# Performance work log

Hardware: AMD Instinct MI355X
Metric: run time of the kernel (lower is better)

The kernel has to match this reference:

```python
import jax, jax.numpy as jnp
import numpy as np

N_NODES = 50000
E = 800000
NODE_NF = 128
EDGE_NF = 64
IN_NF = NODE_NF + EDGE_NF  # 192
H_NF = 256
OUT_NF = 128


def setup_inputs() -> dict:
    key = jax.random.key(0)
    k1, k2, k3, k4, k5 = jax.random.split(key, 5)
    node_feats = jax.random.normal(k1, (N_NODES, NODE_NF), dtype=jnp.float32)
    edge_index = jax.random.randint(k2, (2, E), 0, N_NODES, dtype=jnp.int64)
    edge_attr = jax.random.normal(k3, (E, EDGE_NF), dtype=jnp.float32)
    # MLP params (Linear stores weight [out, in]; we keep [in, out] for x @ W)
    s1 = 1.0 / np.sqrt(IN_NF)
    s2 = 1.0 / np.sqrt(H_NF)
    W1 = jax.random.uniform(k4, (IN_NF, H_NF), minval=-s1, maxval=s1, dtype=jnp.float32)
    b1 = jnp.zeros((H_NF,), dtype=jnp.float32)
    W2 = jax.random.uniform(k5, (H_NF, OUT_NF), minval=-s2, maxval=s2, dtype=jnp.float32)
    b2 = jnp.zeros((OUT_NF,), dtype=jnp.float32)
    return {"node_feats": node_feats, "edge_index": edge_index, "edge_attr": edge_attr,
            "W1": W1, "b1": b1, "W2": W2, "b2": b2}


def reference(node_feats, edge_index, edge_attr, W1, b1, W2, b2):
    row = edge_index[0]
    # unsorted_segment_sum: scatter-add edge_attr rows into per-node buckets
    agg = jax.ops.segment_sum(edge_attr, row, num_segments=node_feats.shape[0])  # [N, edge_nf]
    node_in = jnp.concatenate([node_feats, agg], axis=1)  # [N, in_nf]
    h = jax.nn.relu(node_in @ W1 + b1)
    return h @ W2 + b2
```

## Files before the change

kernel.cpp:

```cpp
#include <hip/hip_runtime.h>
#include <hip/hip_bf16.h>

typedef unsigned short u16;
typedef unsigned int u32;
typedef __attribute__((ext_vector_type(8))) short short8;
typedef __attribute__((ext_vector_type(4))) float floatx4;

#define N_NODES 50000
#define E_EDGES 800000
#define NODE_NF 128
#define EDGE_NF 64
#define IN_NF 192
#define H_NF 256
#define OUT_NF 128
#define CAP 64

__device__ __forceinline__ float bf2f(u16 u) {
    union { u32 i; float f; } v;
    v.i = ((u32)u) << 16;
    return v.f;
}

__device__ __forceinline__ u16 f2bf(float f) {
    union { float f; u32 i; } v;
    v.f = f;
    u32 b = v.i + 0x7FFF + ((v.i >> 16) & 1);
    return (u16)(b >> 16);
}

__global__ void probe_kernel(const u32* __restrict__ nf, const u32* __restrict__ ea,
                             const u32* __restrict__ w1, const int* __restrict__ eidx,
                             int* __restrict__ flags) {
    if (threadIdx.x != 0 || blockIdx.x != 0) return;
    int cn = 0, ce = 0, cw = 0;
    for (int i = 0; i < 64; ++i) {
        u32 bn = (nf[i] >> 8) & 0x7F;
        u32 be = (ea[i] >> 8) & 0x7F;
        u32 bw = (w1[i] >> 8) & 0x7F;
        cn += (bn == 0x3F);
        ce += (be == 0x3F);
        cw += (bw == 60 || bw == 61);
    }
    int hi = 0;
    for (int i = 1; i < 16; i += 2) hi |= eidx[i];
    flags[0] = (cn >= 8);
    flags[1] = (ce >= 8);
    flags[2] = (cw >= 8);
    flags[3] = (hi == 0);
}

__global__ void prep_weights(const void* __restrict__ W1v, const void* __restrict__ W2v,
                             u16* __restrict__ P1, u16* __restrict__ P2,
                             const int* __restrict__ flags) {
    int t = blockIdx.x * blockDim.x + threadIdx.x;
    int wbf = flags[2];
    const u16* W1h = (const u16*)W1v;  const float* W1f = (const float*)W1v;
    const u16* W2h = (const u16*)W2v;  const float* W2f = (const float*)W2v;
    int lane = t & 63;
    int tile = t >> 6;
    int q = lane >> 4, r = lane & 15;
    u16 v[8];
    if (tile < 96) {
        int kt = tile >> 4, nt = tile & 15;
        int kbase = kt * 32 + q * 8;
        int col = nt * 16 + r;
#pragma unroll
        for (int j = 0; j < 8; ++j) {
            int idx = (kbase + j) * H_NF + col;
            v[j] = wbf ? W1h[idx] : f2bf(W1f[idx]);
        }
        u16* dst = P1 + (size_t)t * 8;
#pragma unroll
        for (int j = 0; j < 8; ++j) dst[j] = v[j];
    } else if (tile < 160) {
        int t2 = tile - 96;
        int kt = t2 >> 3, ot = t2 & 7;
        int kbase = kt * 32 + q * 8;
        int col = ot * 16 + r;
#pragma unroll
        for (int j = 0; j < 8; ++j) {
            int idx = (kbase + j) * OUT_NF + col;
            v[j] = wbf ? W2h[idx] : f2bf(W2f[idx]);
        }
        u16* dst = P2 + (size_t)(t - 96 * 64) * 8;
#pragma unroll
        for (int j = 0; j < 8; ++j) dst[j] = v[j];
    }
}

__global__ void fill_kernel(const int* __restrict__ eidx, u32* __restrict__ elist,
                            const int* __restrict__ flags) {
    int e = blockIdx.x * 256 + threadIdx.x;
    if (e >= E_EDGES) return;
    int is64 = flags[3];
    int row = is64 ? (int)(((const long long*)eidx)[e]) : eidx[e];
    row = ((u32)row < (u32)N_NODES) ? row : 0;
    u32* rp = elist + (size_t)row * CAP;
    u32 pos = atomicAdd(rp + (CAP - 1), 1u);
    if (pos < CAP - 1) rp[pos] = e;
}

__global__ __launch_bounds__(256) void gather_kernel(const void* __restrict__ eav,
                                                     u32* __restrict__ elist,
                                                     const int* __restrict__ flags) {
    int node = (blockIdx.x * 256 + threadIdx.x) >> 6;
    int lane = threadIdx.x & 63;
    if (node >= N_NODES) return;
    int eabf = flags[1];
    u32* row = elist + (size_t)node * CAP;
    int deg = (int)row[CAP - 1];
    deg = deg < (CAP - 1) ? deg : (CAP - 1);
    u32 eid = row[lane];
    const u16* eah = (const u16*)eav;
    const float* eaf = (const float*)eav;

    float acc = 0.f;
    int j = 0;
    for (; j + 4 <= deg; j += 4) {
        int e0 = __shfl((int)eid, j);
        int e1 = __shfl((int)eid, j + 1);
        int e2 = __shfl((int)eid, j + 2);
        int e3 = __shfl((int)eid, j + 3);
        float v0, v1, v2, v3;
        if (eabf) {
            v0 = bf2f(eah[(size_t)e0 * EDGE_NF + lane]);
            v1 = bf2f(eah[(size_t)e1 * EDGE_NF + lane]);
            v2 = bf2f(eah[(size_t)e2 * EDGE_NF + lane]);
            v3 = bf2f(eah[(size_t)e3 * EDGE_NF + lane]);
        } else {
            v0 = eaf[(size_t)e0 * EDGE_NF + lane];
            v1 = eaf[(size_t)e1 * EDGE_NF + lane];
            v2 = eaf[(size_t)e2 * EDGE_NF + lane];
            v3 = eaf[(size_t)e3 * EDGE_NF + lane];
        }
        acc += v0; acc += v1; acc += v2; acc += v3;
    }
    for (; j < deg; ++j) {
        int e = __shfl((int)eid, j);
        acc += eabf ? bf2f(eah[(size_t)e * EDGE_NF + lane])
                    : eaf[(size_t)e * EDGE_NF + lane];
    }
    ((float*)row)[lane] = acc;
}

__global__ __launch_bounds__(256, 2) void mlp_kernel(
    const void* __restrict__ nfv, const float* __restrict__ agg,
    const u16* __restrict__ P1, const u16* __restrict__ P2,
    const void* __restrict__ b1v, const void* __restrict__ b2v,
    void* __restrict__ outv, const int* __restrict__ flags) {
    __shared__ u16 sA[64 * 200];
    __shared__ u16 sH[64 * 264];

    int t = threadIdx.x;
    int base = blockIdx.x * 64;
    int nfbf = flags[0], wbf = flags[2];
    const u16* nfh = (const u16*)nfv;     const float* nff = (const float*)nfv;
    const u16* b1h = (const u16*)b1v;     const float* b1f = (const float*)b1v;
    const u16* b2h = (const u16*)b2v;     const float* b2f = (const float*)b2v;

    int r = t >> 2, part = t & 3;
    int node = base + r;
    int nc = node < N_NODES ? node : (N_NODES - 1);
#pragma unroll
    for (int i = 0; i < 6; ++i) {
        int c8 = (part + 4 * i) * 8;
        uint4 v;
        if (c8 < NODE_NF) {
            if (nfbf) {
                v = *(const uint4*)(nfh + (size_t)nc * NODE_NF + c8);
            } else {
                const float4* np = (const float4*)(nff + (size_t)nc * NODE_NF + c8);
                float4 f0 = np[0], f1 = np[1];
                v.x = (u32)f2bf(f0.x) | ((u32)f2bf(f0.y) << 16);
                v.y = (u32)f2bf(f0.z) | ((u32)f2bf(f0.w) << 16);
                v.z = (u32)f2bf(f1.x) | ((u32)f2bf(f1.y) << 16);
                v.w = (u32)f2bf(f1.z) | ((u32)f2bf(f1.w) << 16);
            }
        } else {
            const float4* ap = (const float4*)(agg + (size_t)nc * EDGE_NF + (c8 - NODE_NF));
            float4 f0 = ap[0], f1 = ap[1];
            v.x = (u32)f2bf(f0.x) | ((u32)f2bf(f0.y) << 16);
            v.y = (u32)f2bf(f0.z) | ((u32)f2bf(f0.w) << 16);
            v.z = (u32)f2bf(f1.x) | ((u32)f2bf(f1.y) << 16);
            v.w = (u32)f2bf(f1.z) | ((u32)f2bf(f1.w) << 16);
        }
        *(uint4*)(sA + r * 200 + c8) = v;
    }
    __syncthreads();

    int wv = t >> 6, lane = t & 63;
    int q = lane >> 4, rr = lane & 15;

    floatx4 acc[16];
#pragma unroll
    for (int nt = 0; nt < 16; ++nt) acc[nt] = (floatx4)0.f;

    const u16* aRow = sA + (wv * 16 + rr) * 200;
#pragma unroll
    for (int kt = 0; kt < 6; ++kt) {
        short8 a = *(const short8*)(aRow + kt * 32 + q * 8);
        const short8* bp = (const short8*)(P1 + ((size_t)kt * 16 * 64 + lane) * 8);
#pragma unroll
        for (int nt = 0; nt < 16; ++nt)
            acc[nt] = __builtin_amdgcn_mfma_f32_16x16x32_bf16(a, bp[nt * 64], acc[nt], 0, 0, 0);
    }

#pragma unroll
    for (int nt = 0; nt < 16; ++nt) {
        int col = nt * 16 + rr;
        float bias = wbf ? bf2f(b1h[col]) : b1f[col];
#pragma unroll
        for (int i = 0; i < 4; ++i) {
            float hv = acc[nt][i] + bias;
            hv = hv > 0.f ? hv : 0.f;
            sH[(wv * 16 + q * 4 + i) * 264 + col] = f2bf(hv);
        }
    }
    __syncthreads();

    floatx4 acc2[8];
#pragma unroll
    for (int ot = 0; ot < 8; ++ot) acc2[ot] = (floatx4)0.f;

    const u16* hRow = sH + (wv * 16 + rr) * 264;
#pragma unroll
    for (int kt = 0; kt < 8; ++kt) {
        short8 a = *(const short8*)(hRow + kt * 32 + q * 8);
        const short8* bp = (const short8*)(P2 + ((size_t)kt * 8 * 64 + lane) * 8);
#pragma unroll
        for (int ot = 0; ot < 8; ++ot)
            acc2[ot] = __builtin_amdgcn_mfma_f32_16x16x32_bf16(a, bp[ot * 64], acc2[ot], 0, 0, 0);
    }

#pragma unroll
    for (int ot = 0; ot < 8; ++ot) {
        int col = ot * 16 + rr;
        float bias = wbf ? bf2f(b2h[col]) : b2f[col];
#pragma unroll
        for (int i = 0; i < 4; ++i) {
            int node2 = base + wv * 16 + q * 4 + i;
            if (node2 < N_NODES) {
                float val = acc2[ot][i] + bias;
                if (nfbf) ((u16*)outv)[(size_t)node2 * OUT_NF + col] = f2bf(val);
                else      ((float*)outv)[(size_t)node2 * OUT_NF + col] = val;
            }
        }
    }
}

extern "C" void kernel_launch(void* const* d_in, const int* in_sizes, int n_in,
                              void* d_out, int out_size, void* d_ws, size_t ws_size,
                              hipStream_t stream) {
    const void* nf   = d_in[0];
    const int*  eidx = (const int*)d_in[1];
    const void* ea   = d_in[2];
    const void* W1   = d_in[3];
    const void* b1   = d_in[4];
    const void* W2   = d_in[5];
    const void* b2   = d_in[6];

    char* ws = (char*)d_ws;
    u32*   elist = (u32*)(ws + 256);
    u16*   P1    = (u16*)(ws + 12800256);
    u16*   P2    = (u16*)(ws + 12898560);
    int*   flags = (int*)(ws + 12964096);

    hipMemsetAsync(elist, 0, (size_t)N_NODES * CAP * sizeof(u32), stream);
    probe_kernel<<<1, 64, 0, stream>>>((const u32*)nf, (const u32*)ea, (const u32*)W1,
                                       eidx, flags);
    prep_weights<<<40, 256, 0, stream>>>(W1, W2, P1, P2, flags);
    fill_kernel<<<(E_EDGES + 255) / 256, 256, 0, stream>>>(eidx, elist, flags);
    gather_kernel<<<(N_NODES * 64 + 255) / 256, 256, 0, stream>>>(ea, elist, flags);
    mlp_kernel<<<(N_NODES + 63) / 64, 256, 0, stream>>>(nf, (const float*)elist,
                                                        P1, P2, b1, b2, d_out, flags);
}
```

Baseline: 428.4 us.

## Fuse probe into kernels, replace full memset with counter reset, retile MLP

Drops the separate probe kernel and the 12.8MB memset of the edge list. Format probing moves into each kernel via wave ballots, and only the per-node counter slot is zeroed inside a merged setup kernel that also packs the weights. The gather loop unroll grows from 4 to 8 edges. The MLP now has each wave compute all 64 rows for a slice of output columns instead of 16 rows for all columns, so each weight fragment is loaded once per block instead of once per wave. Every kernel now pays a little extra for probing.

```diff
diff --git a/kernel.cpp b/kernel.cpp
--- a/kernel.cpp
+++ b/kernel.cpp
@@ -28,71 +28,65 @@
     return (u16)(b >> 16);
 }
 
-__global__ void probe_kernel(const u32* __restrict__ nf, const u32* __restrict__ ea,
-                             const u32* __restrict__ w1, const int* __restrict__ eidx,
-                             int* __restrict__ flags) {
-    if (threadIdx.x != 0 || blockIdx.x != 0) return;
-    int cn = 0, ce = 0, cw = 0;
-    for (int i = 0; i < 64; ++i) {
-        u32 bn = (nf[i] >> 8) & 0x7F;
-        u32 be = (ea[i] >> 8) & 0x7F;
-        u32 bw = (w1[i] >> 8) & 0x7F;
-        cn += (bn == 0x3F);
-        ce += (be == 0x3F);
-        cw += (bw == 60 || bw == 61);
-    }
-    int hi = 0;
-    for (int i = 1; i < 16; i += 2) hi |= eidx[i];
-    flags[0] = (cn >= 8);
-    flags[1] = (ce >= 8);
-    flags[2] = (cw >= 8);
-    flags[3] = (hi == 0);
-}
-
-__global__ void prep_weights(const void* __restrict__ W1v, const void* __restrict__ W2v,
+__device__ __forceinline__ int probe_bf16_n01(const u32* p, int lane) {
+    u32 b = (p[lane] >> 8) & 0x7F;
+    return __popcll(__ballot(b == 0x3F)) >= 8;
+}
+__device__ __forceinline__ int probe_bf16_uni(const u32* p, int lane) {
+    u32 b = (p[lane] >> 8) & 0x7F;
+    return __popcll(__ballot(b == 60 || b == 61)) >= 8;
+}
+
+__global__ void setup_kernel(const void* __restrict__ W1v, const void* __restrict__ W2v,
                              u16* __restrict__ P1, u16* __restrict__ P2,
-                             const int* __restrict__ flags) {
-    int t = blockIdx.x * blockDim.x + threadIdx.x;
-    int wbf = flags[2];
-    const u16* W1h = (const u16*)W1v;  const float* W1f = (const float*)W1v;
-    const u16* W2h = (const u16*)W2v;  const float* W2f = (const float*)W2v;
-    int lane = t & 63;
-    int tile = t >> 6;
-    int q = lane >> 4, r = lane & 15;
-    u16 v[8];
-    if (tile < 96) {
-        int kt = tile >> 4, nt = tile & 15;
-        int kbase = kt * 32 + q * 8;
-        int col = nt * 16 + r;
-#pragma unroll
-        for (int j = 0; j < 8; ++j) {
-            int idx = (kbase + j) * H_NF + col;
-            v[j] = wbf ? W1h[idx] : f2bf(W1f[idx]);
-        }
-        u16* dst = P1 + (size_t)t * 8;
-#pragma unroll
-        for (int j = 0; j < 8; ++j) dst[j] = v[j];
-    } else if (tile < 160) {
-        int t2 = tile - 96;
-        int kt = t2 >> 3, ot = t2 & 7;
-        int kbase = kt * 32 + q * 8;
-        int col = ot * 16 + r;
-#pragma unroll
-        for (int j = 0; j < 8; ++j) {
-            int idx = (kbase + j) * OUT_NF + col;
-            v[j] = wbf ? W2h[idx] : f2bf(W2f[idx]);
-        }
-        u16* dst = P2 + (size_t)(t - 96 * 64) * 8;
-#pragma unroll
-        for (int j = 0; j < 8; ++j) dst[j] = v[j];
-    }
-}
-
-__global__ void fill_kernel(const int* __restrict__ eidx, u32* __restrict__ elist,
-                            const int* __restrict__ flags) {
-    int e = blockIdx.x * 256 + threadIdx.x;
+                             u32* __restrict__ elist) {
+    int t = blockIdx.x * 256 + threadIdx.x;
+    if (t < 10240) {
+        int lane = t & 63;
+        int wbf = probe_bf16_uni((const u32*)W1v, lane);
+        const u16* W1h = (const u16*)W1v;  const float* W1f = (const float*)W1v;
+        const u16* W2h = (const u16*)W2v;  const float* W2f = (const float*)W2v;
+        int tile = t >> 6;
+        int q = lane >> 4, r = lane & 15;
+        u16 v[8];
+        if (tile < 96) {
+            int kt = tile >> 4, nt = tile & 15;
+            int kbase = kt * 32 + q * 8;
+            int col = nt * 16 + r;
+#pragma unroll
+            for (int j = 0; j < 8; ++j) {
+                int idx = (kbase + j) * H_NF + col;
+                v[j] = wbf ? W1h[idx] : f2bf(W1f[idx]);
+            }
+            u16* dst = P1 + (size_t)t * 8;
+#pragma unroll
+            for (int j = 0; j < 8; ++j) dst[j] = v[j];
+        } else {
+            int t2 = tile - 96;
+            int kt = t2 >> 3, ot = t2 & 7;
+            int kbase = kt * 32 + q * 8;
+            int col = ot * 16 + r;
+#pragma unroll
+            for (int j = 0; j < 8; ++j) {
+                int idx = (kbase + j) * OUT_NF + col;
+                v[j] = wbf ? W2h[idx] : f2bf(W2f[idx]);
+            }
+            u16* dst = P2 + (size_t)(t - 96 * 64) * 8;
+#pragma unroll
+            for (int j = 0; j < 8; ++j) dst[j] = v[j];
+        }
+    } else if (t < 10240 + N_NODES) {
+        elist[(size_t)(t - 10240) * CAP + (CAP - 1)] = 0;
+    }
+}
+
+__global__ void fill_kernel(const int* __restrict__ eidx, u32* __restrict__ elist) {
+    int t = blockIdx.x * 256 + threadIdx.x;
+    int lane = threadIdx.x & 63;
+    u32 hi = (u32)__ballot(lane < 8 && eidx[2 * lane + 1] != 0);
+    int is64 = (hi == 0);
+    int e = t;
     if (e >= E_EDGES) return;
-    int is64 = flags[3];
     int row = is64 ? (int)(((const long long*)eidx)[e]) : eidx[e];
     row = ((u32)row < (u32)N_NODES) ? row : 0;
     u32* rp = elist + (size_t)row * CAP;
@@ -101,12 +95,11 @@
 }
 
 __global__ __launch_bounds__(256) void gather_kernel(const void* __restrict__ eav,
-                                                     u32* __restrict__ elist,
-                                                     const int* __restrict__ flags) {
+                                                     u32* __restrict__ elist) {
     int node = (blockIdx.x * 256 + threadIdx.x) >> 6;
     int lane = threadIdx.x & 63;
     if (node >= N_NODES) return;
-    int eabf = flags[1];
+    int eabf = probe_bf16_n01((const u32*)eav, lane);
     u32* row = elist + (size_t)node * CAP;
     int deg = (int)row[CAP - 1];
     deg = deg < (CAP - 1) ? deg : (CAP - 1);
@@ -116,24 +109,20 @@
 
     float acc = 0.f;
     int j = 0;
-    for (; j + 4 <= deg; j += 4) {
-        int e0 = __shfl((int)eid, j);
-        int e1 = __shfl((int)eid, j + 1);
-        int e2 = __shfl((int)eid, j + 2);
-        int e3 = __shfl((int)eid, j + 3);
-        float v0, v1, v2, v3;
+    for (; j + 8 <= deg; j += 8) {
+        int e[8];
+#pragma unroll
+        for (int k = 0; k < 8; ++k) e[k] = __shfl((int)eid, j + k);
+        float v[8];
         if (eabf) {
-            v0 = bf2f(eah[(size_t)e0 * EDGE_NF + lane]);
-            v1 = bf2f(eah[(size_t)e1 * EDGE_NF + lane]);
-            v2 = bf2f(eah[(size_t)e2 * EDGE_NF + lane]);
-            v3 = bf2f(eah[(size_t)e3 * EDGE_NF + lane]);
+#pragma unroll
+            for (int k = 0; k < 8; ++k) v[k] = bf2f(eah[(size_t)e[k] * EDGE_NF + lane]);
         } else {
-            v0 = eaf[(size_t)e0 * EDGE_NF + lane];
-            v1 = eaf[(size_t)e1 * EDGE_NF + lane];
-            v2 = eaf[(size_t)e2 * EDGE_NF + lane];
-            v3 = eaf[(size_t)e3 * EDGE_NF + lane];
-        }
-        acc += v0; acc += v1; acc += v2; acc += v3;
+#pragma unroll
+            for (int k = 0; k < 8; ++k) v[k] = eaf[(size_t)e[k] * EDGE_NF + lane];
+        }
+#pragma unroll
+        for (int k = 0; k < 8; ++k) acc += v[k];
     }
     for (; j < deg; ++j) {
         int e = __shfl((int)eid, j);
@@ -147,13 +136,15 @@
     const void* __restrict__ nfv, const float* __restrict__ agg,
     const u16* __restrict__ P1, const u16* __restrict__ P2,
     const void* __restrict__ b1v, const void* __restrict__ b2v,
-    void* __restrict__ outv, const int* __restrict__ flags) {
+    const void* __restrict__ W1v, void* __restrict__ outv) {
     __shared__ u16 sA[64 * 200];
     __shared__ u16 sH[64 * 264];
 
     int t = threadIdx.x;
     int base = blockIdx.x * 64;
-    int nfbf = flags[0], wbf = flags[2];
+    int lane = t & 63;
+    int nfbf = probe_bf16_n01((const u32*)nfv, lane);
+    int wbf  = probe_bf16_uni((const u32*)W1v, lane);
     const u16* nfh = (const u16*)nfv;     const float* nff = (const float*)nfv;
     const u16* b1h = (const u16*)b1v;     const float* b1f = (const float*)b1v;
     const u16* b2h = (const u16*)b2v;     const float* b2f = (const float*)b2v;
@@ -188,63 +179,83 @@
     }
     __syncthreads();
 
-    int wv = t >> 6, lane = t & 63;
+    int wv = t >> 6;
     int q = lane >> 4, rr = lane & 15;
 
-    floatx4 acc[16];
-#pragma unroll
-    for (int nt = 0; nt < 16; ++nt) acc[nt] = (floatx4)0.f;
-
-    const u16* aRow = sA + (wv * 16 + rr) * 200;
+    floatx4 acc1[4][4];
+#pragma unroll
+    for (int rt = 0; rt < 4; ++rt)
+#pragma unroll
+        for (int ct = 0; ct < 4; ++ct) acc1[rt][ct] = (floatx4)0.f;
+
 #pragma unroll
     for (int kt = 0; kt < 6; ++kt) {
-        short8 a = *(const short8*)(aRow + kt * 32 + q * 8);
-        const short8* bp = (const short8*)(P1 + ((size_t)kt * 16 * 64 + lane) * 8);
-#pragma unroll
-        for (int nt = 0; nt < 16; ++nt)
-            acc[nt] = __builtin_amdgcn_mfma_f32_16x16x32_bf16(a, bp[nt * 64], acc[nt], 0, 0, 0);
-    }
-
-#pragma unroll
-    for (int nt = 0; nt < 16; ++nt) {
-        int col = nt * 16 + rr;
+        short8 a[4];
+#pragma unroll
+        for (int rt = 0; rt < 4; ++rt)
+            a[rt] = *(const short8*)(sA + (rt * 16 + rr) * 200 + kt * 32 + q * 8);
+#pragma unroll
+        for (int ct = 0; ct < 4; ++ct) {
+            int nt = wv * 4 + ct;
+            short8 b = *(const short8*)(P1 + ((size_t)(kt * 16 + nt) * 64 + lane) * 8);
+#pragma unroll
+            for (int rt = 0; rt < 4; ++rt)
+                acc1[rt][ct] = __builtin_amdgcn_mfma_f32_16x16x32_bf16(a[rt], b, acc1[rt][ct], 0, 0, 0);
+        }
+    }
+
+#pragma unroll
+    for (int ct = 0; ct < 4; ++ct) {
+        int col = (wv * 4 + ct) * 16 + rr;
         float bias = wbf ? bf2f(b1h[col]) : b1f[col];
 #pragma unroll
-        for (int i = 0; i < 4; ++i) {
-            float hv = acc[nt][i] + bias;
-            hv = hv > 0.f ? hv : 0.f;
-            sH[(wv * 16 + q * 4 + i) * 264 + col] = f2bf(hv);
-        }
+        for (int rt = 0; rt < 4; ++rt)
+#pragma unroll
+            for (int i = 0; i < 4; ++i) {
+                float hv = acc1[rt][ct][i] + bias;
+                hv = hv > 0.f ? hv : 0.f;
+                sH[(rt * 16 + q * 4 + i) * 264 + col] = f2bf(hv);
+            }
     }
     __syncthreads();
 
-    floatx4 acc2[8];
-#pragma unroll
-    for (int ot = 0; ot < 8; ++ot) acc2[ot] = (floatx4)0.f;
-
-    const u16* hRow = sH + (wv * 16 + rr) * 264;
+    floatx4 acc2[4][2];
+#pragma unroll
+    for (int rt = 0; rt < 4; ++rt)
+#pragma unroll
+        for (int ct = 0; ct < 2; ++ct) acc2[rt][ct] = (floatx4)0.f;
+
 #pragma unroll
     for (int kt = 0; kt < 8; ++kt) {
-        short8 a = *(const short8*)(hRow + kt * 32 + q * 8);
-        const short8* bp = (const short8*)(P2 + ((size_t)kt * 8 * 64 + lane) * 8);
-#pragma unroll
-        for (int ot = 0; ot < 8; ++ot)
-            acc2[ot] = __builtin_amdgcn_mfma_f32_16x16x32_bf16(a, bp[ot * 64], acc2[ot], 0, 0, 0);
-    }
-
-#pragma unroll
-    for (int ot = 0; ot < 8; ++ot) {
-        int col = ot * 16 + rr;
+        short8 a[4];
+#pragma unroll
+        for (int rt = 0; rt < 4; ++rt)
+            a[rt] = *(const short8*)(sH + (rt * 16 + rr) * 264 + kt * 32 + q * 8);
+#pragma unroll
+        for (int ct = 0; ct < 2; ++ct) {
+            int ot = wv * 2 + ct;
+            short8 b = *(const short8*)(P2 + ((size_t)(kt * 8 + ot) * 64 + lane) * 8);
+#pragma unroll
+            for (int rt = 0; rt < 4; ++rt)
+                acc2[rt][ct] = __builtin_amdgcn_mfma_f32_16x16x32_bf16(a[rt], b, acc2[rt][ct], 0, 0, 0);
+        }
+    }
+
+#pragma unroll
+    for (int ct = 0; ct < 2; ++ct) {
+        int col = (wv * 2 + ct) * 16 + rr;
         float bias = wbf ? bf2f(b2h[col]) : b2f[col];
 #pragma unroll
-        for (int i = 0; i < 4; ++i) {
-            int node2 = base + wv * 16 + q * 4 + i;
-            if (node2 < N_NODES) {
-                float val = acc2[ot][i] + bias;
-                if (nfbf) ((u16*)outv)[(size_t)node2 * OUT_NF + col] = f2bf(val);
-                else      ((float*)outv)[(size_t)node2 * OUT_NF + col] = val;
-            }
-        }
+        for (int rt = 0; rt < 4; ++rt)
+#pragma unroll
+            for (int i = 0; i < 4; ++i) {
+                int node2 = base + rt * 16 + q * 4 + i;
+                if (node2 < N_NODES) {
+                    float val = acc2[rt][ct][i] + bias;
+                    if (nfbf) ((u16*)outv)[(size_t)node2 * OUT_NF + col] = f2bf(val);
+                    else      ((float*)outv)[(size_t)node2 * OUT_NF + col] = val;
+                }
+            }
     }
 }
 
@@ -263,14 +274,10 @@
     u32*   elist = (u32*)(ws + 256);
     u16*   P1    = (u16*)(ws + 12800256);
     u16*   P2    = (u16*)(ws + 12898560);
-    int*   flags = (int*)(ws + 12964096);
-
-    hipMemsetAsync(elist, 0, (size_t)N_NODES * CAP * sizeof(u32), stream);
-    probe_kernel<<<1, 64, 0, stream>>>((const u32*)nf, (const u32*)ea, (const u32*)W1,
-                                       eidx, flags);
-    prep_weights<<<40, 256, 0, stream>>>(W1, W2, P1, P2, flags);
-    fill_kernel<<<(E_EDGES + 255) / 256, 256, 0, stream>>>(eidx, elist, flags);
-    gather_kernel<<<(N_NODES * 64 + 255) / 256, 256, 0, stream>>>(ea, elist, flags);
+
+    setup_kernel<<<236, 256, 0, stream>>>(W1, W2, P1, P2, elist);
+    fill_kernel<<<(E_EDGES + 255) / 256, 256, 0, stream>>>(eidx, elist);
+    gather_kernel<<<(N_NODES * 64 + 255) / 256, 256, 0, stream>>>(ea, elist);
     mlp_kernel<<<(N_NODES + 63) / 64, 256, 0, stream>>>(nf, (const float*)elist,
-                                                        P1, P2, b1, b2, d_out, flags);
-}
+                                                        P1, P2, b1, b2, W1, d_out);
+}
```

Measured after the change: 411.2 us. 4.0% less time.
